# Performance work log

Measured on AMD Instinct MI355X. Metric: run time of the kernel, lower is better.

Reference implementation:

```python
import jax, jax.numpy as jnp
import numpy as np


def setup_inputs() -> dict:
    key = jax.random.key(0)
    k1, k2 = jax.random.split(key)
    # x: (B, C, D, H, W); w: (out_ch, C * 2*2*2)
    x = jax.random.normal(k1, (4, 64, 33, 33, 33), dtype=jnp.float32)
    w = jax.random.normal(k2, (128, 64 * 8), dtype=jnp.float32) * 0.05
    return {"x": x, "w": w}


def reference(x, w):
    # unfoldNd(kernel=2, stride=1, pad=0) + einsum('ij,kjm->kim', w, patches)
    # is exactly a valid 3D cross-correlation with a 2x2x2 kernel.
    B, C, D, H, W = x.shape
    O = w.shape[0]
    kern = w.reshape(O, C, 2, 2, 2)  # unfold flattening order: (C, kd, kh, kw)
    y = jax.lax.conv_general_dilated(
        x, kern,
        window_strides=(1, 1, 1),
        padding='VALID',
        dimension_numbers=('NCDHW', 'OIDHW', 'NCDHW'),
    )  # (B, O, D-1, H-1, W-1)
    return (y + 1.0) ** 2
```

## Files before the change

kernel.cpp:

```cpp
#include <hip/hip_runtime.h>

typedef __bf16 bf16x8 __attribute__((ext_vector_type(8)));
typedef float f32x4 __attribute__((ext_vector_type(4)));
typedef float f32x16 __attribute__((ext_vector_type(16)));
typedef unsigned short u16;
typedef unsigned int u32;
typedef u32 u32x4 __attribute__((ext_vector_type(4)));
typedef u16 u16x8 __attribute__((ext_vector_type(8)));

#define AS1 __attribute__((address_space(1)))
#define AS3 __attribute__((address_space(3)))
#define GLL16(gp, lp) __builtin_amdgcn_global_load_lds((const AS1 void*)(gp), (AS3 void*)(lp), 16, 0, 0)

__device__ __forceinline__ u16 f32_to_bf16_rne(float f) {
    union { float f; unsigned u; } cv; cv.f = f;
    unsigned u = cv.u;
    return (u16)((u + 0x7FFFu + ((u >> 16) & 1u)) >> 16);
}

__device__ __forceinline__ u32 cvt_pk_bf16(float lo, float hi) {
    u32 r;
    asm("v_cvt_pk_bf16_f32 %0, %1, %2" : "=v"(r) : "v"(lo), "v"(hi));
    return r;
}

__global__ void repack_w4_kernel(const float* __restrict__ w, u16* __restrict__ w4) {
    int e = blockIdx.x * 256 + threadIdx.x;
    int j    = e & 7;
    int half = (e >> 3) & 1;
    int o    = (e >> 4) & 127;
    int cq   = (e >> 11) & 3;
    int koff = (e >> 13) & 7;
    int c = cq * 16 + half * 8 + j;
    w4[e] = f32_to_bf16_rne(w[(o << 9) + (c << 3) + koff]);
}

__global__ void repack_w_kernel(const float* __restrict__ w, u16* __restrict__ w3) {
    int e = blockIdx.x * 256 + threadIdx.x;
    int j    = e & 7;
    int g    = (e >> 3) & 3;
    int o    = (e >> 5) & 127;
    int cb   = (e >> 12) & 1;
    int koff = (e >> 13) & 7;
    int c = (cb << 5) + (g << 3) + j;
    w3[e] = f32_to_bf16_rne(w[(o << 9) + (c << 3) + koff]);
}

__global__ __launch_bounds__(256) void transpose_x_kernel(
    const float* __restrict__ x, u16* __restrict__ xT, u16* __restrict__ x32) {

    const int bid = blockIdx.x;
    const int h = bid % 33;
    const int dq = bid / 33;
    const int d = dq % 33;
    const int b = dq / 33;
    const float* xp = x + (size_t)b * 2299968 + d * 1089 + h * 33;

    const int tid = threadIdx.x;
    const int wv  = tid & 31;
    const int cc  = tid >> 5;
    const float* p = xp + (size_t)cc * 8 * 35937 + wv;
    float f0 = p[0],              f1 = p[35937],          f2 = p[2 * 35937], f3 = p[3 * 35937];
    float f4 = p[(size_t)4*35937],f5 = p[(size_t)5*35937],f6 = p[(size_t)6*35937],f7 = p[(size_t)7*35937];
    u32x4 v;
    v[0] = cvt_pk_bf16(f0, f1);
    v[1] = cvt_pk_bf16(f2, f3);
    v[2] = cvt_pk_bf16(f4, f5);
    v[3] = cvt_pk_bf16(f6, f7);
    *reinterpret_cast<u32x4*>(&xT[(size_t)bid * 2048 + cc * 256 + wv * 8]) = v;

    if (tid < 8) {
        const float* q = xp + (size_t)tid * 8 * 35937 + 32;
        u32x4 m;
        m[0] = cvt_pk_bf16(q[0],              q[35937]);
        m[1] = cvt_pk_bf16(q[2 * 35937],      q[3 * 35937]);
        m[2] = cvt_pk_bf16(q[(size_t)4*35937],q[(size_t)5*35937]);
        m[3] = cvt_pk_bf16(q[(size_t)6*35937],q[(size_t)7*35937]);
        *reinterpret_cast<u32x4*>(&x32[(size_t)bid * 64 + tid * 8]) = m;
    }
}

__global__ __launch_bounds__(512, 4) void conv_mfma_kernel(
    const u16* __restrict__ xT, const u16* __restrict__ x32,
    const u16* __restrict__ w4, float* __restrict__ out) {

    __shared__ __align__(16) u16 xs[19008];

    const int tid = threadIdx.x;
    const int bid = blockIdx.x;
    const int hy0 = (bid & 15) << 1;
    const int dz0 = ((bid >> 4) & 15) << 1;
    const int b   = bid >> 8;

    char* ldsb = (char*)xs;
    const int slab0 = b * 1089 + dz0 * 33 + hy0;
#pragma unroll
    for (int r = 0; r < 5; ++r) {
        if (r == 4 && tid >= 256) continue;
        const int u   = tid + (r << 9);
        const int sid = u >> 8;
        const int s   = (sid * 171) >> 9;
        const int hh  = sid - s * 3;
        const char* src = (const char*)xT + ((size_t)(slab0 + s * 33 + hh) << 12)
                          + ((u & 255) << 4);
        GLL16(src, ldsb + (u << 4));
    }
    if (tid < 72) {
        const int s  = (tid * 171) >> 12;
        const int rr = tid - s * 24;
        const char* src = (const char*)x32
            + ((size_t)(b * 1089 + (dz0 + s) * 33 + hy0) << 7) + (rr << 4);
        GLL16(src, ldsb + 36864 + (tid << 4));
    }
    asm volatile("s_waitcnt vmcnt(0)" ::: "memory");
    __syncthreads();

    const int lane = tid & 63;
    const int l31  = lane & 31;
    const int half = lane >> 5;
    const int wid  = tid >> 6;
    const int o0   = (wid >> 1) << 5;
    const int hrow = wid & 1;

    f32x16 acc[2];
#pragma unroll
    for (int od = 0; od < 2; ++od)
#pragma unroll
        for (int r = 0; r < 16; ++r)
            acc[od][r] = 0.f;

#pragma unroll
    for (int kw = 0; kw < 2; ++kw) {
        const int row = l31 + kw;
#pragma unroll
        for (int cq = 0; cq < 4; ++cq) {
            const int cc = (cq << 1) + half;
            bf16x8 A[2][2];
#pragma unroll
            for (int kd = 0; kd < 2; ++kd)
#pragma unroll
                for (int kh = 0; kh < 2; ++kh) {
                    const int t = (((kd << 2) + (kh << 1) + kw) << 2) + cq;
                    const u16* p = w4 + (t << 11) + ((o0 + l31) << 4) + (half << 3);
                    A[kd][kh] = __builtin_bit_cast(bf16x8, *reinterpret_cast<const u16x8*>(p));
                }
            bf16x8 B[3][2];
#pragma unroll
            for (int s = 0; s < 3; ++s)
#pragma unroll
                for (int kh = 0; kh < 2; ++kh) {
                    const int hh = hrow + kh;
                    const u16* p = (row < 32)
                        ? &xs[((s * 3 + hh) << 11) + (cc << 8) + (row << 3)]
                        : &xs[18432 + s * 192 + hh * 64 + (cc << 3)];
                    B[s][kh] = __builtin_bit_cast(bf16x8, *reinterpret_cast<const u16x8*>(p));
                }
#pragma unroll
            for (int s = 0; s < 3; ++s)
#pragma unroll
                for (int kh = 0; kh < 2; ++kh) {
                    if (s < 2)
                        acc[s] = __builtin_amdgcn_mfma_f32_32x32x16_bf16(
                            A[0][kh], B[s][kh], acc[s], 0, 0, 0);
                    if (s >= 1)
                        acc[s - 1] = __builtin_amdgcn_mfma_f32_32x32x16_bf16(
                            A[1][kh], B[s][kh], acc[s - 1], 0, 0, 0);
                }
        }
    }

    float* ob = out + (size_t)b * 128 * 32768 + ((size_t)dz0 << 10)
                + ((hy0 + hrow) << 5) + l31;
#pragma unroll
    for (int od = 0; od < 2; ++od)
#pragma unroll
        for (int r = 0; r < 16; ++r) {
            const int orow = (r & 3) + ((r >> 2) << 3) + (half << 2);
            float v = acc[od][r] + 1.0f;
            ob[((size_t)(o0 + orow) << 15) + (od << 10)] = v * v;
        }
}

#define XS_ROW 72
__global__ __launch_bounds__(256, 4) void conv_mfma_fallback(
    const float* __restrict__ x, const u16* __restrict__ w3, float* __restrict__ out) {

    __shared__ __align__(16) u16 xs[6 * 33 * XS_ROW];

    const int tid = threadIdx.x;
    const int bid = blockIdx.x;
    const int hy0 = (bid & 15) << 1;
    const int dz  = (bid >> 4) & 31;
    const int b   = bid >> 9;

    const float* xb = x + (size_t)b * 64 * 35937;
    for (int i = tid; i < 1584; i += 256) {
        int w   = i % 33;
        int t   = i / 33;
        int q   = t & 7;
        int kh3 = t >> 3;
        int kd  = kh3 >= 3 ? 1 : 0;
        int kh  = kh3 - kd * 3;
        const float* p = xb + (size_t)(q << 3) * 35937 + (dz + kd) * 1089 + (hy0 + kh) * 33 + w;
        u32x4 v;
        v[0] = cvt_pk_bf16(p[0], p[35937]);
        v[1] = cvt_pk_bf16(p[2 * 35937], p[3 * 35937]);
        v[2] = cvt_pk_bf16(p[4 * 35937], p[5 * 35937]);
        v[3] = cvt_pk_bf16(p[6 * 35937], p[7 * 35937]);
        *reinterpret_cast<u32x4*>(&xs[(kh3 * 33 + w) * XS_ROW + (q << 3)]) = v;
    }
    __syncthreads();

    const int lane = tid & 63;
    const int ln   = lane & 15;
    const int g    = lane >> 4;
    const int n0w  = (tid >> 6) << 5;

    f32x4 acc[2][4];
#pragma unroll
    for (int nf = 0; nf < 2; ++nf)
#pragma unroll
        for (int mf = 0; mf < 4; ++mf)
            acc[nf][mf] = (f32x4){0.f, 0.f, 0.f, 0.f};

#pragma unroll
    for (int cb = 0; cb < 2; ++cb) {
        const int cbase = (cb << 5) + (g << 3);
#pragma unroll
        for (int kd = 0; kd < 2; ++kd) {
            bf16x8 wf[2][4];
#pragma unroll
            for (int nf = 0; nf < 2; ++nf)
#pragma unroll
                for (int kk = 0; kk < 4; ++kk) {
                    const int koff = (kd << 2) + kk;
                    const u16* p = w3 + (size_t)((((koff << 1) + cb) << 7)
                                   + n0w + (nf << 4) + ln) * 32 + (g << 3);
                    wf[nf][kk] = __builtin_bit_cast(bf16x8, *reinterpret_cast<const u16x8*>(p));
                }
#pragma unroll
            for (int kw = 0; kw < 2; ++kw) {
                bf16x8 xf[3][2];
#pragma unroll
                for (int hh = 0; hh < 3; ++hh)
#pragma unroll
                    for (int wh = 0; wh < 2; ++wh) {
                        const int rw = (kd * 3 + hh) * 33 + (wh << 4) + ln + kw;
                        xf[hh][wh] = __builtin_bit_cast(bf16x8,
                            *reinterpret_cast<const u16x8*>(&xs[rw * XS_ROW + cbase]));
                    }
#pragma unroll
                for (int kh = 0; kh < 2; ++kh)
#pragma unroll
                    for (int nf = 0; nf < 2; ++nf)
#pragma unroll
                        for (int mf = 0; mf < 4; ++mf)
                            acc[nf][mf] = __builtin_amdgcn_mfma_f32_16x16x32_bf16(
                                wf[nf][(kh << 1) + kw], xf[(mf >> 1) + kh][mf & 1],
                                acc[nf][mf], 0, 0, 0);
            }
        }
    }

    float* ob = out + ((size_t)b * 128) * 32768 + (dz << 10) + (hy0 << 5);
#pragma unroll
    for (int nf = 0; nf < 2; ++nf)
#pragma unroll
        for (int mf = 0; mf < 4; ++mf) {
            const int wx   = ((mf & 1) << 4) + ln;
            const int hrow = mf >> 1;
            float* o2 = ob + (hrow << 5) + wx;
#pragma unroll
            for (int r = 0; r < 4; ++r) {
                const int n = n0w + (nf << 4) + (g << 2) + r;
                float v = acc[nf][mf][r] + 1.0f;
                o2[(size_t)n << 15] = v * v;
            }
        }
}

extern "C" void kernel_launch(void* const* d_in, const int* in_sizes, int n_in,
                              void* d_out, int out_size, void* d_ws, size_t ws_size,
                              hipStream_t stream) {
    const float* x = (const float*)d_in[0];
    const float* w = (const float*)d_in[1];
    float* out = (float*)d_out;

    const size_t W_BYTES   = 131072;
    const size_t XT_BYTES  = (size_t)4356 * 4096;
    const size_t X32_BYTES = (size_t)4356 * 128;
    const size_t NEED = W_BYTES + XT_BYTES + X32_BYTES;

    if (ws_size >= NEED) {
        u16* w4  = (u16*)d_ws;
        u16* xT  = (u16*)((char*)d_ws + W_BYTES);
        u16* x32 = (u16*)((char*)d_ws + W_BYTES + XT_BYTES);
        repack_w4_kernel<<<256, 256, 0, stream>>>(w, w4);
        transpose_x_kernel<<<4356, 256, 0, stream>>>(x, xT, x32);
        conv_mfma_kernel<<<1024, 512, 0, stream>>>(xT, x32, w4, out);
    } else {
        u16* w3 = (u16*)d_ws;
        repack_w_kernel<<<256, 256, 0, stream>>>(w, w3);
        conv_mfma_fallback<<<2048, 256, 0, stream>>>(x, w3, out);
    }
}
```

Before: 49.55 us.

## Compute four depth slices per block and prefetch next slabs during compute

Each block now covers four output depth slices instead of two, so the grid is halved and LDS grows to hold five input slabs. The block loads three slabs, then issues async global-to-LDS loads for the remaining two while it runs MFMA on the first pair, stores, and then computes the second pair. The aim is to cut redundant halo slab loads and hide global load latency behind compute. The cost is more LDS per block and half as many blocks, which lowers occupancy. The explicit vmcnt wait before the barrier was removed, which risks reading LDS before the async loads have landed.

```diff
diff --git a/kernel.cpp b/kernel.cpp
--- a/kernel.cpp
+++ b/kernel.cpp
@@ -80,20 +80,89 @@
     }
 }
 
+template<int SBASE>
+__device__ __forceinline__ void compute_acc(
+    const u16* __restrict__ xs, const u16* __restrict__ w4,
+    int hrow, int o0, int l31, int half, f32x16 acc[2]) {
+
+#pragma unroll
+    for (int od = 0; od < 2; ++od)
+#pragma unroll
+        for (int r = 0; r < 16; ++r)
+            acc[od][r] = 0.f;
+
+#pragma unroll
+    for (int kw = 0; kw < 2; ++kw) {
+        const int row = l31 + kw;
+#pragma unroll
+        for (int cq = 0; cq < 4; ++cq) {
+            const int cc = (cq << 1) + half;
+            bf16x8 A[2][2];
+#pragma unroll
+            for (int kd = 0; kd < 2; ++kd)
+#pragma unroll
+                for (int kh = 0; kh < 2; ++kh) {
+                    const int t = (((kd << 2) + (kh << 1) + kw) << 2) + cq;
+                    const u16* p = w4 + (t << 11) + ((o0 + l31) << 4) + (half << 3);
+                    A[kd][kh] = __builtin_bit_cast(bf16x8, *reinterpret_cast<const u16x8*>(p));
+                }
+            bf16x8 B[3][2];
+#pragma unroll
+            for (int s = 0; s < 3; ++s)
+#pragma unroll
+                for (int kh = 0; kh < 2; ++kh) {
+                    const int hh = hrow + kh;
+                    const int S  = SBASE + s;
+                    const u16* p = (row < 32)
+                        ? &xs[((S * 3 + hh) << 11) + (cc << 8) + (row << 3)]
+                        : &xs[30720 + S * 192 + hh * 64 + (cc << 3)];
+                    B[s][kh] = __builtin_bit_cast(bf16x8, *reinterpret_cast<const u16x8*>(p));
+                }
+#pragma unroll
+            for (int s = 0; s < 3; ++s)
+#pragma unroll
+                for (int kh = 0; kh < 2; ++kh) {
+                    if (s < 2)
+                        acc[s] = __builtin_amdgcn_mfma_f32_32x32x16_bf16(
+                            A[0][kh], B[s][kh], acc[s], 0, 0, 0);
+                    if (s >= 1)
+                        acc[s - 1] = __builtin_amdgcn_mfma_f32_32x32x16_bf16(
+                            A[1][kh], B[s][kh], acc[s - 1], 0, 0, 0);
+                }
+        }
+    }
+}
+
+__device__ __forceinline__ void store_pair(
+    float* __restrict__ out, const f32x16 acc[2],
+    int b, int dzp, int hy0, int hrow, int o0, int l31, int half) {
+    float* ob = out + (size_t)b * 128 * 32768 + ((size_t)dzp << 10)
+                + ((hy0 + hrow) << 5) + l31;
+#pragma unroll
+    for (int od = 0; od < 2; ++od)
+#pragma unroll
+        for (int r = 0; r < 16; ++r) {
+            const int orow = (r & 3) + ((r >> 2) << 3) + (half << 2);
+            float v = acc[od][r] + 1.0f;
+            ob[((size_t)(o0 + orow) << 15) + (od << 10)] = v * v;
+        }
+}
+
 __global__ __launch_bounds__(512, 4) void conv_mfma_kernel(
     const u16* __restrict__ xT, const u16* __restrict__ x32,
     const u16* __restrict__ w4, float* __restrict__ out) {
 
-    __shared__ __align__(16) u16 xs[19008];
+    __shared__ __align__(16) u16 xs[31680];
 
     const int tid = threadIdx.x;
     const int bid = blockIdx.x;
     const int hy0 = (bid & 15) << 1;
-    const int dz0 = ((bid >> 4) & 15) << 1;
-    const int b   = bid >> 8;
+    const int dz0 = ((bid >> 4) & 7) << 2;
+    const int b   = bid >> 7;
 
     char* ldsb = (char*)xs;
     const int slab0 = b * 1089 + dz0 * 33 + hy0;
+
 #pragma unroll
     for (int r = 0; r < 5; ++r) {
         if (r == 4 && tid >= 256) continue;
@@ -110,10 +179,29 @@
         const int rr = tid - s * 24;
         const char* src = (const char*)x32
             + ((size_t)(b * 1089 + (dz0 + s) * 33 + hy0) << 7) + (rr << 4);
-        GLL16(src, ldsb + 36864 + (tid << 4));
-    }
-    asm volatile("s_waitcnt vmcnt(0)" ::: "memory");
+        GLL16(src, ldsb + 61440 + (tid << 4));
+    }
     __syncthreads();
+
+#pragma unroll
+    for (int r = 0; r < 3; ++r) {
+        const int u   = tid + (r << 9);
+        const int sid = u >> 8;
+        const int sq  = (sid * 171) >> 9;
+        const int hh  = sid - sq * 3;
+        const int S   = 3 + sq;
+        const char* src = (const char*)xT + ((size_t)(slab0 + S * 33 + hh) << 12)
+                          + ((u & 255) << 4);
+        GLL16(src, ldsb + 36864 + (u << 4));
+    }
+    if (tid < 48) {
+        const int sq = (tid * 171) >> 12;
+        const int S  = 3 + sq;
+        const int rr = tid - sq * 24;
+        const char* src = (const char*)x32
+            + ((size_t)(b * 1089 + (dz0 + S) * 33 + hy0) << 7) + (rr << 4);
+        GLL16(src, ldsb + 62592 + (tid << 4));
+    }
 
     const int lane = tid & 63;
     const int l31  = lane & 31;
@@ -122,63 +210,16 @@
     const int o0   = (wid >> 1) << 5;
     const int hrow = wid & 1;
 
-    f32x16 acc[2];
-#pragma unroll
-    for (int od = 0; od < 2; ++od)
-#pragma unroll
-        for (int r = 0; r < 16; ++r)
-            acc[od][r] = 0.f;
-
-#pragma unroll
-    for (int kw = 0; kw < 2; ++kw) {
-        const int row = l31 + kw;
-#pragma unroll
-        for (int cq = 0; cq < 4; ++cq) {
-            const int cc = (cq << 1) + half;
-            bf16x8 A[2][2];
-#pragma unroll
-            for (int kd = 0; kd < 2; ++kd)
-#pragma unroll
-                for (int kh = 0; kh < 2; ++kh) {
-                    const int t = (((kd << 2) + (kh << 1) + kw) << 2) + cq;
-                    const u16* p = w4 + (t << 11) + ((o0 + l31) << 4) + (half << 3);
-                    A[kd][kh] = __builtin_bit_cast(bf16x8, *reinterpret_cast<const u16x8*>(p));
-                }
-            bf16x8 B[3][2];
-#pragma unroll
-            for (int s = 0; s < 3; ++s)
-#pragma unroll
-                for (int kh = 0; kh < 2; ++kh) {
-                    const int hh = hrow + kh;
-                    const u16* p = (row < 32)
-                        ? &xs[((s * 3 + hh) << 11) + (cc << 8) + (row << 3)]
-                        : &xs[18432 + s * 192 + hh * 64 + (cc << 3)];
-                    B[s][kh] = __builtin_bit_cast(bf16x8, *reinterpret_cast<const u16x8*>(p));
-                }
-#pragma unroll
-            for (int s = 0; s < 3; ++s)
-#pragma unroll
-                for (int kh = 0; kh < 2; ++kh) {
-                    if (s < 2)
-                        acc[s] = __builtin_amdgcn_mfma_f32_32x32x16_bf16(
-                            A[0][kh], B[s][kh], acc[s], 0, 0, 0);
-                    if (s >= 1)
-                        acc[s - 1] = __builtin_amdgcn_mfma_f32_32x32x16_bf16(
-                            A[1][kh], B[s][kh], acc[s - 1], 0, 0, 0);
-                }
-        }
-    }
-
-    float* ob = out + (size_t)b * 128 * 32768 + ((size_t)dz0 << 10)
-                + ((hy0 + hrow) << 5) + l31;
-#pragma unroll
-    for (int od = 0; od < 2; ++od)
-#pragma unroll
-        for (int r = 0; r < 16; ++r) {
-            const int orow = (r & 3) + ((r >> 2) << 3) + (half << 2);
-            float v = acc[od][r] + 1.0f;
-            ob[((size_t)(o0 + orow) << 15) + (od << 10)] = v * v;
-        }
+    f32x16 acc0[2];
+    compute_acc<0>(xs, w4, hrow, o0, l31, half, acc0);
+
+    __syncthreads();
+
+    store_pair(out, acc0, b, dz0, hy0, hrow, o0, l31, half);
+
+    f32x16 acc1[2];
+    compute_acc<2>(xs, w4, hrow, o0, l31, half, acc1);
+    store_pair(out, acc1, b, dz0 + 2, hy0, hrow, o0, l31, half);
 }
 
 #define XS_ROW 72
@@ -297,7 +338,7 @@
         u16* x32 = (u16*)((char*)d_ws + W_BYTES + XT_BYTES);
         repack_w4_kernel<<<256, 256, 0, stream>>>(w, w4);
         transpose_x_kernel<<<4356, 256, 0, stream>>>(x, xT, x32);
-        conv_mfma_kernel<<<1024, 512, 0, stream>>>(xT, x32, w4, out);
+        conv_mfma_kernel<<<512, 512, 0, stream>>>(xT, x32, w4, out);
     } else {
         u16* w3 = (u16*)d_ws;
         repack_w_kernel<<<256, 256, 0, stream>>>(w, w3);
```

Measured after the change: 53.63 us. 1.08x slower.

## Merge prepass kernels and retile conv to 1 depth x 8 rows per block

Applied to the files above, without the earlier changes.

Fuses the weight repack and the x transpose into one prepass launch, removing one kernel launch. The conv kernel now tiles 1 depth slice by 8 H rows per block instead of 2x2, with 512 blocks. Each wave computes 4 H rows with 4 accumulators and reuses the B fragment shared between neighbouring rows, which cuts LDS reads and redundant slab loads. Block indices are remapped with an XCD-style swizzle for locality. The cost is doubled LDS per block (about 76KB), which lowers occupancy, and fewer blocks to spread across CUs.

```diff
diff --git a/kernel.cpp b/kernel.cpp
--- a/kernel.cpp
+++ b/kernel.cpp
@@ -24,15 +24,51 @@
     return r;
 }
 
-__global__ void repack_w4_kernel(const float* __restrict__ w, u16* __restrict__ w4) {
-    int e = blockIdx.x * 256 + threadIdx.x;
-    int j    = e & 7;
-    int half = (e >> 3) & 1;
-    int o    = (e >> 4) & 127;
-    int cq   = (e >> 11) & 3;
-    int koff = (e >> 13) & 7;
-    int c = cq * 16 + half * 8 + j;
-    w4[e] = f32_to_bf16_rne(w[(o << 9) + (c << 3) + koff]);
+__global__ __launch_bounds__(256) void prepass_kernel(
+    const float* __restrict__ x, const float* __restrict__ w,
+    u16* __restrict__ xT, u16* __restrict__ x32, u16* __restrict__ w4) {
+
+    const int bid = blockIdx.x;
+    const int tid = threadIdx.x;
+
+    if (bid < 4356) {
+        const int h = bid % 33;
+        const int dq = bid / 33;
+        const int d = dq % 33;
+        const int b = dq / 33;
+        const float* xp = x + (size_t)b * 2299968 + d * 1089 + h * 33;
+
+        const int wv  = tid & 31;
+        const int cc  = tid >> 5;
+        const float* p = xp + (size_t)cc * 8 * 35937 + wv;
+        float f0 = p[0],              f1 = p[35937],          f2 = p[2 * 35937], f3 = p[3 * 35937];
+        float f4 = p[(size_t)4*35937],f5 = p[(size_t)5*35937],f6 = p[(size_t)6*35937],f7 = p[(size_t)7*35937];
+        u32x4 v;
+        v[0] = cvt_pk_bf16(f0, f1);
+        v[1] = cvt_pk_bf16(f2, f3);
+        v[2] = cvt_pk_bf16(f4, f5);
+        v[3] = cvt_pk_bf16(f6, f7);
+        *reinterpret_cast<u32x4*>(&xT[(size_t)bid * 2048 + cc * 256 + wv * 8]) = v;
+
+        if (tid < 8) {
+            const float* q = xp + (size_t)tid * 8 * 35937 + 32;
+            u32x4 m;
+            m[0] = cvt_pk_bf16(q[0],              q[35937]);
+            m[1] = cvt_pk_bf16(q[2 * 35937],      q[3 * 35937]);
+            m[2] = cvt_pk_bf16(q[(size_t)4*35937],q[(size_t)5*35937]);
+            m[3] = cvt_pk_bf16(q[(size_t)6*35937],q[(size_t)7*35937]);
+            *reinterpret_cast<u32x4*>(&x32[(size_t)bid * 64 + tid * 8]) = m;
+        }
+    } else {
+        int e = (bid - 4356) * 256 + tid;
+        int j    = e & 7;
+        int half = (e >> 3) & 1;
+        int o    = (e >> 4) & 127;
+        int cq   = (e >> 11) & 3;
+        int koff = (e >> 13) & 7;
+        int c = cq * 16 + half * 8 + j;
+        w4[e] = f32_to_bf16_rne(w[(o << 9) + (c << 3) + koff]);
+    }
 }
 
 __global__ void repack_w_kernel(const float* __restrict__ w, u16* __restrict__ w3) {
@@ -46,71 +82,38 @@
     w3[e] = f32_to_bf16_rne(w[(o << 9) + (c << 3) + koff]);
 }
 
-__global__ __launch_bounds__(256) void transpose_x_kernel(
-    const float* __restrict__ x, u16* __restrict__ xT, u16* __restrict__ x32) {
-
-    const int bid = blockIdx.x;
-    const int h = bid % 33;
-    const int dq = bid / 33;
-    const int d = dq % 33;
-    const int b = dq / 33;
-    const float* xp = x + (size_t)b * 2299968 + d * 1089 + h * 33;
-
-    const int tid = threadIdx.x;
-    const int wv  = tid & 31;
-    const int cc  = tid >> 5;
-    const float* p = xp + (size_t)cc * 8 * 35937 + wv;
-    float f0 = p[0],              f1 = p[35937],          f2 = p[2 * 35937], f3 = p[3 * 35937];
-    float f4 = p[(size_t)4*35937],f5 = p[(size_t)5*35937],f6 = p[(size_t)6*35937],f7 = p[(size_t)7*35937];
-    u32x4 v;
-    v[0] = cvt_pk_bf16(f0, f1);
-    v[1] = cvt_pk_bf16(f2, f3);
-    v[2] = cvt_pk_bf16(f4, f5);
-    v[3] = cvt_pk_bf16(f6, f7);
-    *reinterpret_cast<u32x4*>(&xT[(size_t)bid * 2048 + cc * 256 + wv * 8]) = v;
-
-    if (tid < 8) {
-        const float* q = xp + (size_t)tid * 8 * 35937 + 32;
-        u32x4 m;
-        m[0] = cvt_pk_bf16(q[0],              q[35937]);
-        m[1] = cvt_pk_bf16(q[2 * 35937],      q[3 * 35937]);
-        m[2] = cvt_pk_bf16(q[(size_t)4*35937],q[(size_t)5*35937]);
-        m[3] = cvt_pk_bf16(q[(size_t)6*35937],q[(size_t)7*35937]);
-        *reinterpret_cast<u32x4*>(&x32[(size_t)bid * 64 + tid * 8]) = m;
-    }
-}
-
 __global__ __launch_bounds__(512, 4) void conv_mfma_kernel(
     const u16* __restrict__ xT, const u16* __restrict__ x32,
     const u16* __restrict__ w4, float* __restrict__ out) {
 
-    __shared__ __align__(16) u16 xs[19008];
-
-    const int tid = threadIdx.x;
-    const int bid = blockIdx.x;
-    const int hy0 = (bid & 15) << 1;
-    const int dz0 = ((bid >> 4) & 15) << 1;
-    const int b   = bid >> 8;
+    __shared__ __align__(16) u16 xs[38016];
+
+    const int tid  = threadIdx.x;
+    const int bid0 = blockIdx.x;
+    const int wgid = ((bid0 & 7) << 6) + (bid0 >> 3);
+    const int b    = wgid >> 7;
+    const int dz   = (wgid >> 2) & 31;
+    const int hy0  = (wgid & 3) << 3;
 
     char* ldsb = (char*)xs;
-    const int slab0 = b * 1089 + dz0 * 33 + hy0;
-#pragma unroll
-    for (int r = 0; r < 5; ++r) {
-        if (r == 4 && tid >= 256) continue;
+    const int slab0 = b * 1089 + dz * 33 + hy0;
+#pragma unroll
+    for (int r = 0; r < 9; ++r) {
         const int u   = tid + (r << 9);
         const int sid = u >> 8;
-        const int s   = (sid * 171) >> 9;
-        const int hh  = sid - s * 3;
-        const char* src = (const char*)xT + ((size_t)(slab0 + s * 33 + hh) << 12)
+        const int kd  = sid >= 9;
+        const int hh  = sid - kd * 9;
+        const char* src = (const char*)xT + ((size_t)(slab0 + kd * 33 + hh) << 12)
                           + ((u & 255) << 4);
         GLL16(src, ldsb + (u << 4));
     }
-    if (tid < 72) {
-        const int s  = (tid * 171) >> 12;
-        const int rr = tid - s * 24;
+    if (tid < 144) {
+        const int sid = tid >> 3;
+        const int kd  = sid >= 9;
+        const int hh  = sid - kd * 9;
         const char* src = (const char*)x32
-            + ((size_t)(b * 1089 + (dz0 + s) * 33 + hy0) << 7) + (rr << 4);
-        GLL16(src, ldsb + 36864 + (tid << 4));
+            + ((size_t)(slab0 + kd * 33 + hh) << 7) + ((tid & 7) << 4);
+        GLL16(src, ldsb + 73728 + (tid << 4));
     }
     asm volatile("s_waitcnt vmcnt(0)" ::: "memory");
     __syncthreads();
@@ -119,15 +122,15 @@
     const int l31  = lane & 31;
     const int half = lane >> 5;
     const int wid  = tid >> 6;
-    const int o0   = (wid >> 1) << 5;
-    const int hrow = wid & 1;
-
-    f32x16 acc[2];
-#pragma unroll
-    for (int od = 0; od < 2; ++od)
+    const int o0   = (wid & 3) << 5;
+    const int hb   = (wid >> 2) << 2;
+
+    f32x16 acc[4];
+#pragma unroll
+    for (int ht = 0; ht < 4; ++ht)
 #pragma unroll
         for (int r = 0; r < 16; ++r)
-            acc[od][r] = 0.f;
+            acc[ht][r] = 0.f;
 
 #pragma unroll
     for (int kw = 0; kw < 2; ++kw) {
@@ -144,41 +147,50 @@
                     const u16* p = w4 + (t << 11) + ((o0 + l31) << 4) + (half << 3);
                     A[kd][kh] = __builtin_bit_cast(bf16x8, *reinterpret_cast<const u16x8*>(p));
                 }
-            bf16x8 B[3][2];
-#pragma unroll
-            for (int s = 0; s < 3; ++s)
-#pragma unroll
-                for (int kh = 0; kh < 2; ++kh) {
-                    const int hh = hrow + kh;
+            bf16x8 Bc[2], Bn[2];
+#pragma unroll
+            for (int kd = 0; kd < 2; ++kd) {
+                const int sid = kd * 9 + hb;
+                const u16* p = (row < 32)
+                    ? &xs[(sid << 11) + (cc << 8) + (row << 3)]
+                    : &xs[36864 + (sid << 6) + (cc << 3)];
+                Bc[kd] = __builtin_bit_cast(bf16x8, *reinterpret_cast<const u16x8*>(p));
+            }
+#pragma unroll
+            for (int ht = 0; ht < 4; ++ht) {
+#pragma unroll
+                for (int kd = 0; kd < 2; ++kd) {
+                    const int sid = kd * 9 + hb + ht + 1;
                     const u16* p = (row < 32)
-                        ? &xs[((s * 3 + hh) << 11) + (cc << 8) + (row << 3)]
-                        : &xs[18432 + s * 192 + hh * 64 + (cc << 3)];
-                    B[s][kh] = __builtin_bit_cast(bf16x8, *reinterpret_cast<const u16x8*>(p));
+                        ? &xs[(sid << 11) + (cc << 8) + (row << 3)]
+                        : &xs[36864 + (sid << 6) + (cc << 3)];
+                    Bn[kd] = __builtin_bit_cast(bf16x8, *reinterpret_cast<const u16x8*>(p));
                 }
 #pragma unroll
-            for (int s = 0; s < 3; ++s)
-#pragma unroll
-                for (int kh = 0; kh < 2; ++kh) {
-                    if (s < 2)
-                        acc[s] = __builtin_amdgcn_mfma_f32_32x32x16_bf16(
-                            A[0][kh], B[s][kh], acc[s], 0, 0, 0);
-                    if (s >= 1)
-                        acc[s - 1] = __builtin_amdgcn_mfma_f32_32x32x16_bf16(
-                            A[1][kh], B[s][kh], acc[s - 1], 0, 0, 0);
+                for (int kd = 0; kd < 2; ++kd) {
+                    acc[ht] = __builtin_amdgcn_mfma_f32_32x32x16_bf16(
+                        A[kd][0], Bc[kd], acc[ht], 0, 0, 0);
+                    acc[ht] = __builtin_amdgcn_mfma_f32_32x32x16_bf16(
+                        A[kd][1], Bn[kd], acc[ht], 0, 0, 0);
                 }
-        }
-    }
-
-    float* ob = out + (size_t)b * 128 * 32768 + ((size_t)dz0 << 10)
-                + ((hy0 + hrow) << 5) + l31;
-#pragma unroll
-    for (int od = 0; od < 2; ++od)
-#pragma unroll
-        for (int r = 0; r < 16; ++r) {
-            const int orow = (r & 3) + ((r >> 2) << 3) + (half << 2);
-            float v = acc[od][r] + 1.0f;
-            ob[((size_t)(o0 + orow) << 15) + (od << 10)] = v * v;
-        }
+                Bc[0] = Bn[0];
+                Bc[1] = Bn[1];
+            }
+        }
+    }
+
+    float* ob = out + (size_t)b * 128 * 32768 + ((size_t)dz << 10)
+                + ((hy0 + hb) << 5) + l31;
+#pragma unroll
+    for (int r = 0; r < 16; ++r) {
+        const int orow = (r & 3) + ((r >> 2) << 3) + (half << 2);
+        float* o2 = ob + ((size_t)(o0 + orow) << 15);
+#pragma unroll
+        for (int ht = 0; ht < 4; ++ht) {
+            float v = acc[ht][r] + 1.0f;
+            o2[ht << 5] = v * v;
+        }
+    }
 }
 
 #define XS_ROW 72
@@ -295,9 +307,8 @@
         u16* w4  = (u16*)d_ws;
         u16* xT  = (u16*)((char*)d_ws + W_BYTES);
         u16* x32 = (u16*)((char*)d_ws + W_BYTES + XT_BYTES);
-        repack_w4_kernel<<<256, 256, 0, stream>>>(w, w4);
-        transpose_x_kernel<<<4356, 256, 0, stream>>>(x, xT, x32);
-        conv_mfma_kernel<<<1024, 512, 0, stream>>>(xT, x32, w4, out);
+        prepass_kernel<<<4612, 256, 0, stream>>>(x, w, xT, x32, w4);
+        conv_mfma_kernel<<<512, 512, 0, stream>>>(xT, x32, w4, out);
     } else {
         u16* w3 = (u16*)d_ws;
         repack_w_kernel<<<256, 256, 0, stream>>>(w, w3);
```

After: 43.61 us. 12.0% less time.
